# Kernel optimization log

Measured on AMD Instinct MI355X. Metric: run time of the kernel, lower is better.

## Reference

```python
import jax, jax.numpy as jnp
import numpy as np

B, S, A, C, E, H = 256, 512, 8, 256, 64, 256

def _lin_params(key, din, dout):
    k1, k2 = jax.random.split(key)
    bound = 1.0 / np.sqrt(din)
    w = jax.random.uniform(k1, (din, dout), minval=-bound, maxval=bound, dtype=jnp.float32)
    b = jax.random.uniform(k2, (dout,), minval=-bound, maxval=bound, dtype=jnp.float32)
    return w, b

def setup_inputs() -> dict:
    key = jax.random.key(0)
    ks = jax.random.split(key, 9)
    q = jax.random.normal(ks[0], (B, S, A), dtype=jnp.float32)
    st = jax.random.normal(ks[1], (B, S, C), dtype=jnp.float32)
    w1a, b1a = _lin_params(ks[2], C, H)
    w1b, b1b = _lin_params(ks[3], H, A * E)
    w2a, b2a = _lin_params(ks[4], C, H)
    w2b, b2b = _lin_params(ks[5], H, E)
    wb1, bb1 = _lin_params(ks[6], C, E)
    wb2a, bb2a = _lin_params(ks[7], C, H)
    wb2b, bb2b = _lin_params(ks[8], H, 1)
    return dict(agent_q_values=q, central_states=st,
                w1a=w1a, b1a=b1a, w1b=w1b, b1b=b1b,
                w2a=w2a, b2a=b2a, w2b=w2b, b2b=b2b,
                wb1=wb1, bb1=bb1,
                wb2a=wb2a, bb2a=bb2a, wb2b=wb2b, bb2b=bb2b)

def _mlp(x, wa, ba, wb, bb):
    # Linear -> ELU -> Linear
    h = jax.nn.elu(x @ wa + ba)
    return h @ wb + bb

def reference(agent_q_values, central_states,
              w1a, b1a, w1b, b1b,
              w2a, b2a, w2b, b2b,
              wb1, bb1,
              wb2a, bb2a, wb2b, bb2b):
    bsz, seq, na = agent_q_values.shape
    st = central_states.reshape(-1, C)                      # [N, C]
    q = agent_q_values.reshape(-1, na)                      # [N, A]
    w1 = jnp.abs(_mlp(st, w1a, b1a, w1b, b1b)).reshape(-1, na, E)   # [N, A, E]
    b1 = st @ wb1 + bb1                                     # [N, E]
    w2 = jnp.abs(_mlp(st, w2a, b2a, w2b, b2b))              # [N, E]
    b2 = _mlp(st, wb2a, bb2a, wb2b, bb2b)                   # [N, 1]
    hidden = jax.nn.relu(jnp.einsum('na,nae->ne', q, w1) + b1)      # [N, E]
    joint = jnp.einsum('ne,ne->n', hidden, w2)[:, None] + b2        # [N, 1]
    return joint.reshape(bsz, seq, 1)
```

## Files before the change

### kernel.cpp

```cpp
#include <hip/hip_runtime.h>
#include <math.h>

typedef __bf16 bf16_t;
typedef bf16_t bf16x8 __attribute__((ext_vector_type(8)));
typedef float  floatx4 __attribute__((ext_vector_type(4)));

#define MFMA16(a, b, c) __builtin_amdgcn_mfma_f32_16x16x32_bf16((a), (b), (c), 0, 0, 0)

constexpr int NTOT = 256 * 512;
constexpr int CDIM = 256;

constexpr int N_TILES  = 88;
constexpr int WS_ELEMS = N_TILES * 4096;

__global__ void prep_weights(const float* __restrict__ w1a, const float* __restrict__ w1b,
                             const float* __restrict__ w2a, const float* __restrict__ w2b,
                             const float* __restrict__ wb1, const float* __restrict__ wb2a,
                             bf16_t* __restrict__ ws) {
  int idx = blockIdx.x * 256 + threadIdx.x;
  if (idx >= WS_ELEMS) return;
  int t   = idx >> 12;
  int rel = idx & 4095;
  const float* src; int dout; int ct;
  if      (t < 16) { src = w1a;  dout = 256; ct = t; }
  else if (t < 20) { src = wb1;  dout = 64;  ct = t - 16; }
  else if (t < 52) { src = w1b;  dout = 512; ct = t - 20; }
  else if (t < 68) { src = w2a;  dout = 256; ct = t - 52; }
  else if (t < 72) { src = w2b;  dout = 64;  ct = t - 68; }
  else             { src = wb2a; dout = 256; ct = t - 72; }
  int j    = rel & 7;
  int lane = (rel >> 3) & 63;
  int ks   = rel >> 9;
  int o = ct * 16 + (lane & 15);
  int k = ks * 32 + (lane >> 4) * 8 + j;
  ws[idx] = (bf16_t)src[(size_t)k * dout + o];
}

__device__ __forceinline__ void gload_lds16(const bf16_t* g, bf16_t* l) {
  __builtin_amdgcn_global_load_lds(
      (const __attribute__((address_space(1))) unsigned int*)g,
      (__attribute__((address_space(3))) unsigned int*)l, 16, 0, 0);
}

__global__ __launch_bounds__(256, 2)
void mixing_fused(const float* __restrict__ q,
                  const float* __restrict__ st,
                  const bf16_t* __restrict__ W,
                  const float* __restrict__ b1a, const float* __restrict__ b1b,
                  const float* __restrict__ b2a, const float* __restrict__ b2b,
                  const float* __restrict__ bb1,
                  const float* __restrict__ bb2a,
                  const float* __restrict__ wb2b, const float* __restrict__ bb2b,
                  float* __restrict__ out) {
  __shared__ __align__(16) bf16_t wbuf[2][8192];
  __shared__ __align__(16) bf16_t t_s[4][2][32][36];
  __shared__ __align__(16) float  q_s[4][256];

  const int tid  = threadIdx.x;
  const int wid  = tid >> 6;
  const int lane = tid & 63;
  const int l15  = lane & 15;
  const int quad = lane >> 4;
  const int m0   = blockIdx.x * 128 + wid * 32;

  auto stage = [&](int g) {
    const bf16_t* src = W + (size_t)g * 8192 + wid * 2048 + lane * 8;
    bf16_t* dst = &wbuf[g & 1][wid * 2048];
#pragma unroll
    for (int i = 0; i < 4; ++i)
      gload_lds16(src + i * 512, dst + i * 512);
  };

  *(float4*)&q_s[wid][lane * 4] = *(const float4*)(q + (size_t)m0 * 8 + lane * 4);

  bf16x8 sA[2][8];
#pragma unroll
  for (int rt = 0; rt < 2; ++rt) {
    const float* rp = st + (size_t)(m0 + rt * 16 + l15) * CDIM;
#pragma unroll
    for (int ks = 0; ks < 8; ++ks) {
      int k0 = ks * 32 + quad * 8;
      float4 f0 = *(const float4*)(rp + k0);
      float4 f1 = *(const float4*)(rp + k0 + 4);
      bf16x8 v;
      v[0] = (bf16_t)f0.x; v[1] = (bf16_t)f0.y; v[2] = (bf16_t)f0.z; v[3] = (bf16_t)f0.w;
      v[4] = (bf16_t)f1.x; v[5] = (bf16_t)f1.y; v[6] = (bf16_t)f1.z; v[7] = (bf16_t)f1.w;
      sA[rt][ks] = v;
    }
  }

  auto gemmL = [&](int buf, int h, const bf16x8 (&A)[2][8], floatx4 (&acc)[2]) {
    floatx4 z = {0.f, 0.f, 0.f, 0.f};
    acc[0] = z; acc[1] = z;
#pragma unroll
    for (int kk = 0; kk < 8; ++kk) {
      bf16x8 b = *(const bf16x8*)&wbuf[buf][h * 4096 + kk * 512 + lane * 8];
      acc[0] = MFMA16(A[0][kk], b, acc[0]);
      acc[1] = MFMA16(A[1][kk], b, acc[1]);
    }
  };

  stage(0);

  bf16x8 hA[2][8];

#pragma unroll
  for (int ks = 0; ks < 8; ++ks) {
    __syncthreads();
    stage(ks + 1);
    const int buf = ks & 1;
#pragma unroll
    for (int h = 0; h < 2; ++h) {
      int ct = 2 * ks + h;
      floatx4 acc[2];
      gemmL(buf, h, sA, acc);
      float bias = b1a[ct * 16 + l15];
#pragma unroll
      for (int rt = 0; rt < 2; ++rt)
#pragma unroll
        for (int i = 0; i < 4; ++i) {
          float v = acc[rt][i] + bias;
          v = v > 0.f ? v : (__expf(v) - 1.f);
          t_s[wid][buf][rt * 16 + quad * 4 + i][h * 16 + l15] = (bf16_t)v;
        }
    }
#pragma unroll
    for (int rt = 0; rt < 2; ++rt)
      hA[rt][ks] = *(const bf16x8*)&t_s[wid][buf][rt * 16 + l15][quad * 8];
  }

  floatx4 hid[2][4];
#pragma unroll
  for (int gg = 0; gg < 2; ++gg) {
    __syncthreads();
    stage(9 + gg);
    const int buf = gg & 1;
#pragma unroll
    for (int h = 0; h < 2; ++h) {
      int et = 2 * gg + h;
      floatx4 acc[2];
      gemmL(buf, h, sA, acc);
      float bias = bb1[et * 16 + l15];
      hid[0][et] = acc[0] + bias;
      hid[1][et] = acc[1] + bias;
    }
  }

#pragma unroll 1
  for (int a = 0; a < 8; ++a) {
#pragma unroll
    for (int g2 = 0; g2 < 2; ++g2) {
      const int idx = a * 2 + g2;
      __syncthreads();
      stage(11 + idx);
      const int buf = g2;
#pragma unroll
      for (int h = 0; h < 2; ++h) {
        int ct = a * 4 + g2 * 2 + h;
        const int et = g2 * 2 + h;
        floatx4 acc[2];
        gemmL(buf, h, hA, acc);
        float bias = b1b[ct * 16 + l15];
#pragma unroll
        for (int rt = 0; rt < 2; ++rt)
#pragma unroll
          for (int i = 0; i < 4; ++i) {
            float w1v = fabsf(acc[rt][i] + bias);
            float qv  = q_s[wid][(rt * 16 + quad * 4 + i) * 8 + a];
            hid[rt][et][i] += qv * w1v;
          }
      }
    }
  }
#pragma unroll
  for (int rt = 0; rt < 2; ++rt)
#pragma unroll
    for (int et = 0; et < 4; ++et)
#pragma unroll
      for (int i = 0; i < 4; ++i) hid[rt][et][i] = fmaxf(hid[rt][et][i], 0.f);

#pragma unroll
  for (int ks = 0; ks < 8; ++ks) {
    __syncthreads();
    stage(27 + ks);
    const int buf = ks & 1;
#pragma unroll
    for (int h = 0; h < 2; ++h) {
      int ct = 2 * ks + h;
      floatx4 acc[2];
      gemmL(buf, h, sA, acc);
      float bias = b2a[ct * 16 + l15];
#pragma unroll
      for (int rt = 0; rt < 2; ++rt)
#pragma unroll
        for (int i = 0; i < 4; ++i) {
          float v = acc[rt][i] + bias;
          v = v > 0.f ? v : (__expf(v) - 1.f);
          t_s[wid][buf][rt * 16 + quad * 4 + i][h * 16 + l15] = (bf16_t)v;
        }
    }
#pragma unroll
    for (int rt = 0; rt < 2; ++rt)
      hA[rt][ks] = *(const bf16x8*)&t_s[wid][buf][rt * 16 + l15][quad * 8];
  }

  float pj[2][4] = {{0.f, 0.f, 0.f, 0.f}, {0.f, 0.f, 0.f, 0.f}};
#pragma unroll
  for (int gg = 0; gg < 2; ++gg) {
    __syncthreads();
    stage(35 + gg);
    const int buf = gg & 1;
#pragma unroll
    for (int h = 0; h < 2; ++h) {
      int et = 2 * gg + h;
      floatx4 acc[2];
      gemmL(buf, h, hA, acc);
      float bias = b2b[et * 16 + l15];
#pragma unroll
      for (int rt = 0; rt < 2; ++rt)
#pragma unroll
        for (int i = 0; i < 4; ++i) {
          float w2v = fabsf(acc[rt][i] + bias);
          pj[rt][i] += hid[rt][et][i] * w2v;
        }
    }
  }

  float pb[2][4] = {{0.f, 0.f, 0.f, 0.f}, {0.f, 0.f, 0.f, 0.f}};
#pragma unroll 1
  for (int gg = 0; gg < 8; ++gg) {
    __syncthreads();
    if (gg < 7) stage(37 + gg);
    const int buf = gg & 1;
#pragma unroll
    for (int h = 0; h < 2; ++h) {
      int ct = 2 * gg + h;
      floatx4 acc[2];
      gemmL(buf, h, sA, acc);
      float bias = bb2a[ct * 16 + l15];
      float wv   = wb2b[ct * 16 + l15];
#pragma unroll
      for (int rt = 0; rt < 2; ++rt)
#pragma unroll
        for (int i = 0; i < 4; ++i) {
          float v = acc[rt][i] + bias;
          v = v > 0.f ? v : (__expf(v) - 1.f);
          pb[rt][i] += v * wv;
        }
    }
  }

  float bb2 = bb2b[0];
#pragma unroll
  for (int rt = 0; rt < 2; ++rt)
#pragma unroll
    for (int i = 0; i < 4; ++i) {
      float v = pj[rt][i] + pb[rt][i];
      v += __shfl_xor(v, 1);
      v += __shfl_xor(v, 2);
      v += __shfl_xor(v, 4);
      v += __shfl_xor(v, 8);
      if (l15 == 0) out[m0 + rt * 16 + quad * 4 + i] = v + bb2;
    }
}

extern "C" void kernel_launch(void* const* d_in, const int* in_sizes, int n_in,
                              void* d_out, int out_size, void* d_ws, size_t ws_size,
                              hipStream_t stream) {
  const float* q    = (const float*)d_in[0];
  const float* st   = (const float*)d_in[1];
  const float* w1a  = (const float*)d_in[2];
  const float* b1a  = (const float*)d_in[3];
  const float* w1b  = (const float*)d_in[4];
  const float* b1b  = (const float*)d_in[5];
  const float* w2a  = (const float*)d_in[6];
  const float* b2a  = (const float*)d_in[7];
  const float* w2b  = (const float*)d_in[8];
  const float* b2b  = (const float*)d_in[9];
  const float* wb1  = (const float*)d_in[10];
  const float* bb1  = (const float*)d_in[11];
  const float* wb2a = (const float*)d_in[12];
  const float* bb2a = (const float*)d_in[13];
  const float* wb2b = (const float*)d_in[14];
  const float* bb2b = (const float*)d_in[15];
  bf16_t* W = (bf16_t*)d_ws;

  hipLaunchKernelGGL(prep_weights, dim3((WS_ELEMS + 255) / 256), dim3(256), 0, stream,
                     w1a, w1b, w2a, w2b, wb1, wb2a, W);
  hipLaunchKernelGGL(mixing_fused, dim3(NTOT / 128), dim3(256), 0, stream,
                     q, st, W, b1a, b1b, b2a, b2b, bb1, bb2a, wb2b, bb2b, (float*)d_out);
}
```

Baseline: 330.9 us.

## Halve rows per wave to cut registers and raise occupancy

Each wave now handles 16 rows instead of 32, so the A fragments, hidden accumulators and activations shrink to half. Launch bounds rise from 2 to 4 blocks per CU, the grid doubles, and the staging buffer for intermediate activations loses its double buffer. The goal is more resident waves to hide latency. In exchange every block restages the full weight set for half as many rows, doubling weight traffic into LDS, and each B-fragment load from LDS now feeds one MFMA instead of two.

Measured after the change: 320.3 us. 3.2% less time.

```diff
diff --git a/kernel.cpp b/kernel.cpp
--- a/kernel.cpp
+++ b/kernel.cpp
@@ -42,7 +42,7 @@
       (__attribute__((address_space(3))) unsigned int*)l, 16, 0, 0);
 }
 
-__global__ __launch_bounds__(256, 2)
+__global__ __launch_bounds__(256, 4)
 void mixing_fused(const float* __restrict__ q,
                   const float* __restrict__ st,
                   const bf16_t* __restrict__ W,
@@ -53,15 +53,15 @@
                   const float* __restrict__ wb2b, const float* __restrict__ bb2b,
                   float* __restrict__ out) {
   __shared__ __align__(16) bf16_t wbuf[2][8192];
-  __shared__ __align__(16) bf16_t t_s[4][2][32][36];
-  __shared__ __align__(16) float  q_s[4][256];
+  __shared__ __align__(16) bf16_t t_s[4][16][36];
+  __shared__ __align__(16) float  q_s[4][128];
 
   const int tid  = threadIdx.x;
   const int wid  = tid >> 6;
   const int lane = tid & 63;
   const int l15  = lane & 15;
   const int quad = lane >> 4;
-  const int m0   = blockIdx.x * 128 + wid * 32;
+  const int m0   = blockIdx.x * 64 + wid * 16;
 
   auto stage = [&](int g) {
     const bf16_t* src = W + (size_t)g * 8192 + wid * 2048 + lane * 8;
@@ -71,12 +71,11 @@
       gload_lds16(src + i * 512, dst + i * 512);
   };
 
-  *(float4*)&q_s[wid][lane * 4] = *(const float4*)(q + (size_t)m0 * 8 + lane * 4);
-
-  bf16x8 sA[2][8];
-#pragma unroll
-  for (int rt = 0; rt < 2; ++rt) {
-    const float* rp = st + (size_t)(m0 + rt * 16 + l15) * CDIM;
+  *(float2*)&q_s[wid][lane * 2] = *(const float2*)(q + (size_t)m0 * 8 + lane * 2);
+
+  bf16x8 sA[8];
+  {
+    const float* rp = st + (size_t)(m0 + l15) * CDIM;
 #pragma unroll
     for (int ks = 0; ks < 8; ++ks) {
       int k0 = ks * 32 + quad * 8;
@@ -85,24 +84,23 @@
       bf16x8 v;
       v[0] = (bf16_t)f0.x; v[1] = (bf16_t)f0.y; v[2] = (bf16_t)f0.z; v[3] = (bf16_t)f0.w;
       v[4] = (bf16_t)f1.x; v[5] = (bf16_t)f1.y; v[6] = (bf16_t)f1.z; v[7] = (bf16_t)f1.w;
-      sA[rt][ks] = v;
-    }
-  }
-
-  auto gemmL = [&](int buf, int h, const bf16x8 (&A)[2][8], floatx4 (&acc)[2]) {
+      sA[ks] = v;
+    }
+  }
+
+  auto gemmL = [&](int buf, int h, const bf16x8 (&A)[8], floatx4& acc) {
     floatx4 z = {0.f, 0.f, 0.f, 0.f};
-    acc[0] = z; acc[1] = z;
+    acc = z;
 #pragma unroll
     for (int kk = 0; kk < 8; ++kk) {
       bf16x8 b = *(const bf16x8*)&wbuf[buf][h * 4096 + kk * 512 + lane * 8];
-      acc[0] = MFMA16(A[0][kk], b, acc[0]);
-      acc[1] = MFMA16(A[1][kk], b, acc[1]);
+      acc = MFMA16(A[kk], b, acc);
     }
   };
 
   stage(0);
 
-  bf16x8 hA[2][8];
+  bf16x8 hA[8];
 
 #pragma unroll
   for (int ks = 0; ks < 8; ++ks) {
@@ -112,24 +110,20 @@
 #pragma unroll
     for (int h = 0; h < 2; ++h) {
       int ct = 2 * ks + h;
-      floatx4 acc[2];
+      floatx4 acc;
       gemmL(buf, h, sA, acc);
       float bias = b1a[ct * 16 + l15];
 #pragma unroll
-      for (int rt = 0; rt < 2; ++rt)
-#pragma unroll
-        for (int i = 0; i < 4; ++i) {
-          float v = acc[rt][i] + bias;
-          v = v > 0.f ? v : (__expf(v) - 1.f);
-          t_s[wid][buf][rt * 16 + quad * 4 + i][h * 16 + l15] = (bf16_t)v;
-        }
-    }
-#pragma unroll
-    for (int rt = 0; rt < 2; ++rt)
-      hA[rt][ks] = *(const bf16x8*)&t_s[wid][buf][rt * 16 + l15][quad * 8];
-  }
-
-  floatx4 hid[2][4];
+      for (int i = 0; i < 4; ++i) {
+        float v = acc[i] + bias;
+        v = v > 0.f ? v : (__expf(v) - 1.f);
+        t_s[wid][quad * 4 + i][h * 16 + l15] = (bf16_t)v;
+      }
+    }
+    hA[ks] = *(const bf16x8*)&t_s[wid][l15][quad * 8];
+  }
+
+  floatx4 hid[4];
 #pragma unroll
   for (int gg = 0; gg < 2; ++gg) {
     __syncthreads();
@@ -138,16 +132,19 @@
 #pragma unroll
     for (int h = 0; h < 2; ++h) {
       int et = 2 * gg + h;
-      floatx4 acc[2];
+      floatx4 acc;
       gemmL(buf, h, sA, acc);
       float bias = bb1[et * 16 + l15];
-      hid[0][et] = acc[0] + bias;
-      hid[1][et] = acc[1] + bias;
+      hid[et] = acc + bias;
     }
   }
 
 #pragma unroll 1
   for (int a = 0; a < 8; ++a) {
+    float qv[4];
+#pragma unroll
+    for (int i = 0; i < 4; ++i)
+      qv[i] = q_s[wid][(quad * 4 + i) * 8 + a];
 #pragma unroll
     for (int g2 = 0; g2 < 2; ++g2) {
       const int idx = a * 2 + g2;
@@ -158,26 +155,21 @@
       for (int h = 0; h < 2; ++h) {
         int ct = a * 4 + g2 * 2 + h;
         const int et = g2 * 2 + h;
-        floatx4 acc[2];
+        floatx4 acc;
         gemmL(buf, h, hA, acc);
         float bias = b1b[ct * 16 + l15];
 #pragma unroll
-        for (int rt = 0; rt < 2; ++rt)
-#pragma unroll
-          for (int i = 0; i < 4; ++i) {
-            float w1v = fabsf(acc[rt][i] + bias);
-            float qv  = q_s[wid][(rt * 16 + quad * 4 + i) * 8 + a];
-            hid[rt][et][i] += qv * w1v;
-          }
-      }
-    }
-  }
-#pragma unroll
-  for (int rt = 0; rt < 2; ++rt)
-#pragma unroll
-    for (int et = 0; et < 4; ++et)
-#pragma unroll
-      for (int i = 0; i < 4; ++i) hid[rt][et][i] = fmaxf(hid[rt][et][i], 0.f);
+        for (int i = 0; i < 4; ++i) {
+          float w1v = fabsf(acc[i] + bias);
+          hid[et][i] += qv[i] * w1v;
+        }
+      }
+    }
+  }
+#pragma unroll
+  for (int et = 0; et < 4; ++et)
+#pragma unroll
+    for (int i = 0; i < 4; ++i) hid[et][i] = fmaxf(hid[et][i], 0.f);
 
 #pragma unroll
   for (int ks = 0; ks < 8; ++ks) {
@@ -187,24 +179,20 @@
 #pragma unroll
     for (int h = 0; h < 2; ++h) {
       int ct = 2 * ks + h;
-      floatx4 acc[2];
+      floatx4 acc;
       gemmL(buf, h, sA, acc);
       float bias = b2a[ct * 16 + l15];
 #pragma unroll
-      for (int rt = 0; rt < 2; ++rt)
-#pragma unroll
-        for (int i = 0; i < 4; ++i) {
-          float v = acc[rt][i] + bias;
-          v = v > 0.f ? v : (__expf(v) - 1.f);
-          t_s[wid][buf][rt * 16 + quad * 4 + i][h * 16 + l15] = (bf16_t)v;
-        }
-    }
-#pragma unroll
-    for (int rt = 0; rt < 2; ++rt)
-      hA[rt][ks] = *(const bf16x8*)&t_s[wid][buf][rt * 16 + l15][quad * 8];
-  }
-
-  float pj[2][4] = {{0.f, 0.f, 0.f, 0.f}, {0.f, 0.f, 0.f, 0.f}};
+      for (int i = 0; i < 4; ++i) {
+        float v = acc[i] + bias;
+        v = v > 0.f ? v : (__expf(v) - 1.f);
+        t_s[wid][quad * 4 + i][h * 16 + l15] = (bf16_t)v;
+      }
+    }
+    hA[ks] = *(const bf16x8*)&t_s[wid][l15][quad * 8];
+  }
+
+  float p[4] = {0.f, 0.f, 0.f, 0.f};
 #pragma unroll
   for (int gg = 0; gg < 2; ++gg) {
     __syncthreads();
@@ -213,20 +201,17 @@
 #pragma unroll
     for (int h = 0; h < 2; ++h) {
       int et = 2 * gg + h;
-      floatx4 acc[2];
+      floatx4 acc;
       gemmL(buf, h, hA, acc);
       float bias = b2b[et * 16 + l15];
 #pragma unroll
-      for (int rt = 0; rt < 2; ++rt)
-#pragma unroll
-        for (int i = 0; i < 4; ++i) {
-          float w2v = fabsf(acc[rt][i] + bias);
-          pj[rt][i] += hid[rt][et][i] * w2v;
-        }
-    }
-  }
-
-  float pb[2][4] = {{0.f, 0.f, 0.f, 0.f}, {0.f, 0.f, 0.f, 0.f}};
+      for (int i = 0; i < 4; ++i) {
+        float w2v = fabsf(acc[i] + bias);
+        p[i] += hid[et][i] * w2v;
+      }
+    }
+  }
+
 #pragma unroll 1
   for (int gg = 0; gg < 8; ++gg) {
     __syncthreads();
@@ -235,33 +220,29 @@
 #pragma unroll
     for (int h = 0; h < 2; ++h) {
       int ct = 2 * gg + h;
-      floatx4 acc[2];
+      floatx4 acc;
       gemmL(buf, h, sA, acc);
       float bias = bb2a[ct * 16 + l15];
       float wv   = wb2b[ct * 16 + l15];
 #pragma unroll
-      for (int rt = 0; rt < 2; ++rt)
-#pragma unroll
-        for (int i = 0; i < 4; ++i) {
-          float v = acc[rt][i] + bias;
-          v = v > 0.f ? v : (__expf(v) - 1.f);
-          pb[rt][i] += v * wv;
-        }
+      for (int i = 0; i < 4; ++i) {
+        float v = acc[i] + bias;
+        v = v > 0.f ? v : (__expf(v) - 1.f);
+        p[i] += v * wv;
+      }
     }
   }
 
   float bb2 = bb2b[0];
 #pragma unroll
-  for (int rt = 0; rt < 2; ++rt)
-#pragma unroll
-    for (int i = 0; i < 4; ++i) {
-      float v = pj[rt][i] + pb[rt][i];
-      v += __shfl_xor(v, 1);
-      v += __shfl_xor(v, 2);
-      v += __shfl_xor(v, 4);
-      v += __shfl_xor(v, 8);
-      if (l15 == 0) out[m0 + rt * 16 + quad * 4 + i] = v + bb2;
-    }
+  for (int i = 0; i < 4; ++i) {
+    float v = p[i];
+    v += __shfl_xor(v, 1);
+    v += __shfl_xor(v, 2);
+    v += __shfl_xor(v, 4);
+    v += __shfl_xor(v, 8);
+    if (l15 == 0) out[m0 + quad * 4 + i] = v + bb2;
+  }
 }
 
 extern "C" void kernel_launch(void* const* d_in, const int* in_sizes, int n_in,
@@ -287,6 +268,6 @@
 
   hipLaunchKernelGGL(prep_weights, dim3((WS_ELEMS + 255) / 256), dim3(256), 0, stream,
                      w1a, w1b, w2a, w2b, wb1, wb2a, W);
-  hipLaunchKernelGGL(mixing_fused, dim3(NTOT / 128), dim3(256), 0, stream,
+  hipLaunchKernelGGL(mixing_fused, dim3(NTOT / 64), dim3(256), 0, stream,
                      q, st, W, b1a, b1b, b2a, b2b, bb1, bb2a, wb2b, bb2b, (float*)d_out);
 }
```
